# Kernel tuning notes

Hardware: AMD Instinct MI355X
Metric: run time of the kernel (lower is better)

Reference implementation:

```python
import jax, jax.numpy as jnp
import numpy as np
from jax import lax


def setup_inputs() -> dict:
    key = jax.random.key(0)
    k1, k2 = jax.random.split(key)
    B, C, H, W = 4, 64, 64, 64
    foreground = jax.random.normal(k1, (B, C, H, W), dtype=jnp.float32)
    masks = jax.random.uniform(k2, (B, 1, H, W), dtype=jnp.float32)
    return {"foreground": foreground, "masks": masks}


def reference(foreground, masks):
    # First-call path of KnowledgeConsistentAttention (att_scores_prev is None).
    # patch_size=3 -> padding=1 around 1x1 dynamic kernels; propagate_size=3 -> 3x3 sum pool.
    B, C, H, W = foreground.shape
    P = H * W
    # Dynamic 1x1 kernels: one per spatial location, L2-normalized over channels.
    K = foreground.reshape(B, C, P).transpose(0, 2, 1)            # [B, P, C]
    norm = jnp.sqrt(jnp.sum(K * K, axis=2, keepdims=True))        # flatten(1).norm per kernel
    K = K / (norm + 1e-8)
    # conv2d with 1x1 kernels and padding=1 == GEMM over zero-padded input.
    Xpad = jnp.pad(foreground, ((0, 0), (0, 0), (1, 1), (1, 1)))  # [B, C, H+2, W+2]
    scores = jnp.einsum('bpc,bchw->bphw', K, Xpad)                # [B, P, H+2, W+2]
    # avg_pool2d(k=3, stride=1, pad=1) * 9 == zero-padded 3x3 sum pool.
    scores = lax.reduce_window(scores, jnp.float32(0.0), lax.add,
                               (1, 1, 3, 3), (1, 1, 1, 1), 'SAME')
    attn = jax.nn.softmax(scores, axis=1)                          # softmax over P kernels
    # conv_transpose2d with 1x1 kernels, padding=1 crops the border back to HxW.
    out = jnp.einsum('bphw,bpc->bchw', attn[:, :, 1:-1, 1:-1], K)  # [B, C, H, W]
    return out
```

## Files before the change

kernel.cpp:

```cpp
#include <hip/hip_runtime.h>
#include <hip/hip_bf16.h>
#include <math.h>

#define Bn 4
#define Cn 64
#define Pn 4096
#define QT 64
#define PBK 128
#define NITER (Pn / PBK)
#define LOG2E 1.4426950408889634f

#define STG_BUF 32768
#define SL_OFF  98304
#define SMEM_BYTES 106496

typedef __attribute__((ext_vector_type(8))) short short8;
typedef __attribute__((ext_vector_type(4))) short short4v;
typedef __attribute__((ext_vector_type(4))) float float4v;
typedef unsigned short bfu;

__device__ __forceinline__ bfu f2bf(float x) {
    unsigned u = __float_as_uint(x);
    u = (u + 0x7fffu + ((u >> 16) & 1u)) >> 16;
    return (bfu)u;
}

__device__ __forceinline__ void gl16(const bfu* g, void* l) {
    __builtin_amdgcn_global_load_lds(
        (const __attribute__((address_space(1))) void*)g,
        (__attribute__((address_space(3))) void*)l, 16, 0, 0);
}

__global__ __launch_bounds__(256) void prep_kernel(const float* __restrict__ fg,
                                                   bfu* __restrict__ Kpc,
                                                   bfu* __restrict__ Kcp2,
                                                   float* __restrict__ S) {
    __shared__ float shbuf[64 * 64];
    int t = threadIdx.x;
    if (blockIdx.x < 512) {
        float* tile  = shbuf;
        float* rnorm = shbuf + 64 * 33;
        int b  = blockIdx.x >> 7;
        int p0 = (blockIdx.x & 127) << 5;
        const float* src = fg + (size_t)b * Cn * Pn + p0;
        #pragma unroll
        for (int i = 0; i < 8; ++i) {
            int idx = i * 256 + t;
            int c = idx >> 5, p = idx & 31;
            tile[c * 33 + p] = src[(size_t)c * Pn + p];
        }
        __syncthreads();
        if (t < 32) {
            float ss = 0.f;
            #pragma unroll
            for (int c = 0; c < 64; ++c) { float v = tile[c * 33 + t]; ss += v * v; }
            rnorm[t] = 1.0f / (sqrtf(ss) + 1e-8f);
        }
        __syncthreads();
        bfu* dpc = Kpc + ((size_t)b * Pn + p0) * Cn;
        #pragma unroll
        for (int i = 0; i < 8; ++i) {
            int idx = i * 256 + t;
            int p = idx >> 6, c = idx & 63;
            dpc[(size_t)p * Cn + c] = f2bf(tile[c * 33 + p] * rnorm[p]);
        }
        bfu* d2 = Kcp2 + ((size_t)b * 256 + (p0 >> 4)) * 1024;
        #pragma unroll
        for (int i = 0; i < 8; ++i) {
            int idx = i * 256 + t;
            int c = idx >> 5, p = idx & 31;
            d2[(size_t)(p >> 4) * 1024 + c * 16 + (p & 15)] =
                f2bf(tile[c * 33 + p] * rnorm[p]);
        }
    } else {
        float (*pl)[64] = (float(*)[64])shbuf;
        int bc = blockIdx.x - 512;
        const float* src = fg + (size_t)bc * Pn;
        float*       dst = S  + (size_t)bc * Pn;
        #pragma unroll
        for (int i = 0; i < 16; ++i) {
            int idx = i * 256 + t;
            pl[idx >> 6][idx & 63] = src[idx];
        }
        __syncthreads();
        #pragma unroll
        for (int i = 0; i < 16; ++i) {
            int idx = i * 256 + t;
            int h = idx >> 6, w = idx & 63;
            float s = 0.f;
            #pragma unroll
            for (int dh = -1; dh <= 1; ++dh) {
                int hh = h + dh;
                if (hh < 0 || hh >= 64) continue;
                #pragma unroll
                for (int dw = -1; dw <= 1; ++dw) {
                    int ww = w + dw;
                    if (ww < 0 || ww >= 64) continue;
                    s += pl[hh][ww];
                }
            }
            dst[idx] = s * LOG2E;
        }
    }
}

__global__ __launch_bounds__(512, 1) void flash_kernel(const bfu* __restrict__ Kpc,
                                                       const bfu* __restrict__ Kcp2,
                                                       const float* __restrict__ S,
                                                       float* __restrict__ out) {
    __shared__ __align__(16) unsigned char smem[SMEM_BYTES];
    __shared__ float wredl[8][QT];
    bfu* Sl = (bfu*)(smem + SL_OFF);

    int i  = blockIdx.x;
    int b  = (i & 7) >> 1;
    int qt = ((i >> 3) << 1) | (i & 1);
    int q0 = qt * QT;
    int t  = threadIdx.x;
    int w = t >> 6, l = t & 63, lq = l & 15, quad = l >> 4;

    const float* Sg  = S    + (size_t)b * Cn * Pn;
    const bfu*   gpc = Kpc  + (size_t)b * Pn * Cn;
    const bfu*   gt  = Kcp2 + (size_t)b * 256 * 1024;

    {
        int c = t >> 3, qq = (t & 7) * 8;
        const float* sp = &Sg[(size_t)c * Pn + q0 + qq];
        float4 v0 = *(const float4*)sp;
        float4 v1 = *(const float4*)(sp + 4);
        float vv[8] = {v0.x, v0.y, v0.z, v0.w, v1.x, v1.y, v1.z, v1.w};
        int ch = c >> 3, cl = c & 7;
        #pragma unroll
        for (int k = 0; k < 8; ++k) {
            int row = qq + k;
            Sl[row * 64 + ((ch ^ (row & 7)) << 3) + cl] = f2bf(vv[k]);
        }
    }
    __syncthreads();

    short8 bs[4][2];
    #pragma unroll
    for (int nt = 0; nt < 4; ++nt)
        #pragma unroll
        for (int ks = 0; ks < 2; ++ks) {
            int row = nt * 16 + lq;
            bs[nt][ks] = *(const short8*)&Sl[row * 64 + (((ks * 4 + quad) ^ (lq & 7)) << 3)];
        }

    float4v o[4][4];
    #pragma unroll
    for (int nt = 0; nt < 4; ++nt)
        #pragma unroll
        for (int cb = 0; cb < 4; ++cb) o[nt][cb] = (float4v){0.f, 0.f, 0.f, 0.f};
    float lacc[4] = {0.f, 0.f, 0.f, 0.f};

    int l8 = l >> 3, l7 = l & 7;
    int aoff = l8 * 64 + (((l7 ^ l8)) << 3);
    int toff = l * 8;
    int abyte0 = lq * 128 + (((quad)     ^ (lq & 7)) << 4);
    int abyte1 = lq * 128 + (((4 + quad) ^ (lq & 7)) << 4);
    int tbyte  = 16384 + lq * 32 + quad * 8;

    unsigned wb = (unsigned)w * 2048;
    unsigned ro = 0 * STG_BUF, mo = 1 * STG_BUF, io = 2 * STG_BUF;

    #define ISSUE(tile, boff)                                                      \
    {                                                                              \
        const bfu* gA = gpc + ((size_t)(tile) * PBK + (size_t)w * 16) * 64;        \
        const bfu* gT = gt + ((size_t)(tile) * 8 + w) * 1024;                      \
        gl16(gA + aoff,       smem + (boff) + wb);                                 \
        gl16(gA + 512 + aoff, smem + (boff) + wb + 1024);                          \
        gl16(gT + toff,       smem + (boff) + 16384 + wb);                         \
        gl16(gT + 512 + toff, smem + (boff) + 16384 + wb + 1024);                  \
    }

    ISSUE(0, ro);
    ISSUE(1, mo);

    for (int pb = 0; pb < NITER; ++pb) {
        if (pb < NITER - 2) {
            ISSUE(pb + 2, io);
            asm volatile("s_waitcnt vmcnt(8)" ::: "memory");
        } else if (pb == NITER - 2) {
            asm volatile("s_waitcnt vmcnt(4)" ::: "memory");
        } else {
            asm volatile("s_waitcnt vmcnt(0)" ::: "memory");
        }

        short8 af0 = *(const short8*)(smem + ro + wb + abyte0);
        short8 af1 = *(const short8*)(smem + ro + wb + abyte1);
        short4v kb[4];
        #pragma unroll
        for (int cb = 0; cb < 4; ++cb)
            kb[cb] = *(const short4v*)(smem + ro + wb * 0 + (unsigned)w * 2048 + tbyte + cb * 512);

        float4v sc[4];
        #pragma unroll
        for (int nt = 0; nt < 4; ++nt) {
            float4v acc = (float4v){0.f, 0.f, 0.f, 0.f};
            acc = __builtin_amdgcn_mfma_f32_16x16x32_bf16(af0, bs[nt][0], acc, 0, 0, 0);
            acc = __builtin_amdgcn_mfma_f32_16x16x32_bf16(af1, bs[nt][1], acc, 0, 0, 0);
            sc[nt] = acc;
        }

        short4v epk[4];
        #pragma unroll
        for (int nt = 0; nt < 4; ++nt) {
            float e0 = __builtin_amdgcn_exp2f(sc[nt][0]);
            float e1 = __builtin_amdgcn_exp2f(sc[nt][1]);
            float e2 = __builtin_amdgcn_exp2f(sc[nt][2]);
            float e3 = __builtin_amdgcn_exp2f(sc[nt][3]);
            lacc[nt] += (e0 + e1) + (e2 + e3);
            short4v ep = {(short)f2bf(e0), (short)f2bf(e1), (short)f2bf(e2), (short)f2bf(e3)};
            epk[nt] = ep;
        }

        #pragma unroll
        for (int cb = 0; cb < 4; ++cb) {
            #pragma unroll
            for (int nt = 0; nt < 4; ++nt)
                o[nt][cb] = __builtin_amdgcn_mfma_f32_16x16x16bf16_1k(epk[nt], kb[cb], o[nt][cb], 0, 0, 0);
        }

        unsigned tmp = ro; ro = mo; mo = io; io = tmp;
    }
    #undef ISSUE

    #pragma unroll
    for (int nt = 0; nt < 4; ++nt) {
        lacc[nt] += __shfl_xor(lacc[nt], 16);
        lacc[nt] += __shfl_xor(lacc[nt], 32);
    }
    if (quad == 0)
        #pragma unroll
        for (int nt = 0; nt < 4; ++nt) wredl[w][nt * 16 + lq] = lacc[nt];

    float* Ol = (float*)smem;
    __syncthreads();
    if (w < 4) {
        #pragma unroll
        for (int nt = 0; nt < 4; ++nt)
            #pragma unroll
            for (int cb = 0; cb < 4; ++cb)
                #pragma unroll
                for (int r = 0; r < 4; ++r)
                    Ol[(w * 64 + 16 * cb + lq) * 66 + nt * 16 + quad * 4 + r] = o[nt][cb][r];
    }
    __syncthreads();
    if (w >= 4) {
        #pragma unroll
        for (int nt = 0; nt < 4; ++nt)
            #pragma unroll
            for (int cb = 0; cb < 4; ++cb)
                #pragma unroll
                for (int r = 0; r < 4; ++r)
                    Ol[((w - 4) * 64 + 16 * cb + lq) * 66 + nt * 16 + quad * 4 + r] += o[nt][cb][r];
    }
    __syncthreads();

    float* og = out + (size_t)b * Cn * Pn;
    #pragma unroll
    for (int k = 0; k < 8; ++k) {
        int idx = k * 512 + t;
        int c = idx >> 6, q = idx & 63;
        float lsum = ((wredl[0][q] + wredl[1][q]) + (wredl[2][q] + wredl[3][q])) +
                     ((wredl[4][q] + wredl[5][q]) + (wredl[6][q] + wredl[7][q]));
        float v = ((Ol[c * 66 + q] + Ol[(64 + c) * 66 + q]) +
                   (Ol[(128 + c) * 66 + q] + Ol[(192 + c) * 66 + q])) / lsum;
        og[(size_t)c * Pn + q0 + q] = v;
    }
}

extern "C" void kernel_launch(void* const* d_in, const int* in_sizes, int n_in,
                              void* d_out, int out_size, void* d_ws, size_t ws_size,
                              hipStream_t stream) {
    const float* fg = (const float*)d_in[0];
    float* out = (float*)d_out;
    bfu*   Kpc  = (bfu*)d_ws;
    bfu*   Kcp2 = Kpc + (size_t)Bn * Pn * Cn;
    float* S    = (float*)(Kcp2 + (size_t)Bn * Pn * Cn);

    prep_kernel <<<768, 256, 0, stream>>>(fg, Kpc, Kcp2, S);
    flash_kernel<<<Bn * 64, 512, 0, stream>>>(Kpc, Kcp2, S, out);
}
```

Baseline: 94.90 us.

## Deepen LDS pipeline to four stages and prefetch fragments into registers

Moves from a three-buffer to a four-buffer global-to-LDS ring, which raises LDS use to about 136KB. The LDS fragments for the next tile are now read one iteration early into registers, so their latency overlaps the current tile's MFMAs. It also raises wave priority around the MFMA blocks and replaces the software bf16 rounding with the hardware packed v_cvt_pk_bf16_f32 instruction. The cost is higher register pressure from the double-buffered fragments, and the larger LDS footprint may lower occupancy.

```diff
diff --git a/kernel.cpp b/kernel.cpp
--- a/kernel.cpp
+++ b/kernel.cpp
@@ -11,12 +11,13 @@
 #define LOG2E 1.4426950408889634f
 
 #define STG_BUF 32768
-#define SL_OFF  98304
-#define SMEM_BYTES 106496
+#define SL_OFF  131072
+#define SMEM_BYTES 139264
 
 typedef __attribute__((ext_vector_type(8))) short short8;
 typedef __attribute__((ext_vector_type(4))) short short4v;
 typedef __attribute__((ext_vector_type(4))) float float4v;
+typedef __attribute__((ext_vector_type(2))) unsigned uint2v;
 typedef unsigned short bfu;
 
 __device__ __forceinline__ bfu f2bf(float x) {
@@ -155,14 +156,13 @@
     float lacc[4] = {0.f, 0.f, 0.f, 0.f};
 
     int l8 = l >> 3, l7 = l & 7;
-    int aoff = l8 * 64 + (((l7 ^ l8)) << 3);
+    int aoff = l8 * 64 + ((l7 ^ l8) << 3);
     int toff = l * 8;
     int abyte0 = lq * 128 + (((quad)     ^ (lq & 7)) << 4);
     int abyte1 = lq * 128 + (((4 + quad) ^ (lq & 7)) << 4);
     int tbyte  = 16384 + lq * 32 + quad * 8;
 
     unsigned wb = (unsigned)w * 2048;
-    unsigned ro = 0 * STG_BUF, mo = 1 * STG_BUF, io = 2 * STG_BUF;
 
     #define ISSUE(tile, boff)                                                      \
     {                                                                              \
@@ -174,34 +174,48 @@
         gl16(gT + 512 + toff, smem + (boff) + 16384 + wb + 1024);                  \
     }
 
-    ISSUE(0, ro);
-    ISSUE(1, mo);
+    ISSUE(0, 0u);
+    ISSUE(1, STG_BUF);
+    ISSUE(2, 2u * STG_BUF);
+    asm volatile("s_waitcnt vmcnt(8)" ::: "memory");
+    short8 af0c = *(const short8*)(smem + wb + abyte0);
+    short8 af1c = *(const short8*)(smem + wb + abyte1);
+    short4v kbc[4];
+    #pragma unroll
+    for (int cb = 0; cb < 4; ++cb)
+        kbc[cb] = *(const short4v*)(smem + wb + tbyte + cb * 512);
 
     for (int pb = 0; pb < NITER; ++pb) {
-        if (pb < NITER - 2) {
-            ISSUE(pb + 2, io);
+        if (pb + 3 < NITER) {
+            ISSUE(pb + 3, (unsigned)((pb + 3) & 3) * STG_BUF);
             asm volatile("s_waitcnt vmcnt(8)" ::: "memory");
+        } else if (pb == NITER - 3) {
+            asm volatile("s_waitcnt vmcnt(4)" ::: "memory");
         } else if (pb == NITER - 2) {
-            asm volatile("s_waitcnt vmcnt(4)" ::: "memory");
-        } else {
             asm volatile("s_waitcnt vmcnt(0)" ::: "memory");
         }
 
-        short8 af0 = *(const short8*)(smem + ro + wb + abyte0);
-        short8 af1 = *(const short8*)(smem + ro + wb + abyte1);
-        short4v kb[4];
-        #pragma unroll
-        for (int cb = 0; cb < 4; ++cb)
-            kb[cb] = *(const short4v*)(smem + ro + wb * 0 + (unsigned)w * 2048 + tbyte + cb * 512);
+        short8 af0n, af1n;
+        short4v kbn[4];
+        if (pb + 1 < NITER) {
+            unsigned nb = (unsigned)((pb + 1) & 3) * STG_BUF;
+            af0n = *(const short8*)(smem + nb + wb + abyte0);
+            af1n = *(const short8*)(smem + nb + wb + abyte1);
+            #pragma unroll
+            for (int cb = 0; cb < 4; ++cb)
+                kbn[cb] = *(const short4v*)(smem + nb + wb + tbyte + cb * 512);
+        }
 
         float4v sc[4];
+        __builtin_amdgcn_s_setprio(1);
         #pragma unroll
         for (int nt = 0; nt < 4; ++nt) {
             float4v acc = (float4v){0.f, 0.f, 0.f, 0.f};
-            acc = __builtin_amdgcn_mfma_f32_16x16x32_bf16(af0, bs[nt][0], acc, 0, 0, 0);
-            acc = __builtin_amdgcn_mfma_f32_16x16x32_bf16(af1, bs[nt][1], acc, 0, 0, 0);
+            acc = __builtin_amdgcn_mfma_f32_16x16x32_bf16(af0c, bs[nt][0], acc, 0, 0, 0);
+            acc = __builtin_amdgcn_mfma_f32_16x16x32_bf16(af1c, bs[nt][1], acc, 0, 0, 0);
             sc[nt] = acc;
         }
+        __builtin_amdgcn_s_setprio(0);
 
         short4v epk[4];
         #pragma unroll
@@ -211,18 +225,27 @@
             float e2 = __builtin_amdgcn_exp2f(sc[nt][2]);
             float e3 = __builtin_amdgcn_exp2f(sc[nt][3]);
             lacc[nt] += (e0 + e1) + (e2 + e3);
-            short4v ep = {(short)f2bf(e0), (short)f2bf(e1), (short)f2bf(e2), (short)f2bf(e3)};
-            epk[nt] = ep;
-        }
-
+            unsigned plo, phi;
+            asm("v_cvt_pk_bf16_f32 %0, %1, %2" : "=v"(plo) : "v"(e0), "v"(e1));
+            asm("v_cvt_pk_bf16_f32 %0, %1, %2" : "=v"(phi) : "v"(e2), "v"(e3));
+            uint2v pk2 = {plo, phi};
+            epk[nt] = __builtin_bit_cast(short4v, pk2);
+        }
+
+        __builtin_amdgcn_s_setprio(1);
         #pragma unroll
         for (int cb = 0; cb < 4; ++cb) {
             #pragma unroll
             for (int nt = 0; nt < 4; ++nt)
-                o[nt][cb] = __builtin_amdgcn_mfma_f32_16x16x16bf16_1k(epk[nt], kb[cb], o[nt][cb], 0, 0, 0);
-        }
-
-        unsigned tmp = ro; ro = mo; mo = io; io = tmp;
+                o[nt][cb] = __builtin_amdgcn_mfma_f32_16x16x16bf16_1k(epk[nt], kbc[cb], o[nt][cb], 0, 0, 0);
+        }
+        __builtin_amdgcn_s_setprio(0);
+
+        if (pb + 1 < NITER) {
+            af0c = af0n; af1c = af1n;
+            #pragma unroll
+            for (int cb = 0; cb < 4; ++cb) kbc[cb] = kbn[cb];
+        }
     }
     #undef ISSUE
 
```

Measured after the change: 94.52 us. Within noise of the previous version (-0.4%).
